# Performance work log

Measured on AMD Instinct MI355X. Metric: run time of the kernel, lower is better.

Reference implementation:

```python
import jax, jax.numpy as jnp
import numpy as np

K, N, E, D = 4, 2048, 4096, 128
BETA = 0.6
EPS = 0.01           # epsilon in hard-sigmoid gating
LAM = 0.05           # lambda_schedule
TC0, TCMAX = 0.3, 0.7
COS_EPS = 1e-8       # F.cosine_similarity eps
MAX_SCORED_EDGES = 500
EDGE_DENSITY = 0.008


def setup_inputs() -> dict:
    key = jax.random.key(0)
    ks = jax.random.split(key, 8)
    s = 0.02
    H = (jax.random.uniform(ks[0], (K, N, E)) < EDGE_DENSITY).astype(jnp.float32)
    X = jax.random.normal(ks[1], (N, D), jnp.float32)
    return dict(
        H=H, X=X, epoch=50,
        mlp_w1=jax.random.normal(ks[2], (K, D, D), jnp.float32) * s,
        mlp_b1=jnp.zeros((K, D), jnp.float32),
        mlp_w2=jax.random.normal(ks[3], (K, D, D), jnp.float32) * s,
        mlp_b2=jnp.zeros((K, D), jnp.float32),
        comp_W=jax.random.normal(ks[4], (K, D, D), jnp.float32) * 0.01,
        att_w1=jax.random.normal(ks[5], (K, D, D // 2), jnp.float32) * s,
        att_b1=jnp.zeros((K, D // 2), jnp.float32),
        att_w2=jax.random.normal(ks[6], (K, D // 2, 1), jnp.float32) * s,
        att_b2=jnp.zeros((K, 1), jnp.float32),
    )


def reference(H, X, epoch, mlp_w1, mlp_b1, mlp_w2, mlp_b2, comp_W,
              att_w1, att_b1, att_w2, att_b2):
    # ---- component level (Eq. 4, batched over K) ----
    h1 = jax.nn.relu(jnp.einsum('nd,kdh->knh', X, mlp_w1) + mlp_b1[:, None, :])
    Xk = jnp.einsum('knh,khe->kne', h1, mlp_w2) + mlp_b2[:, None, :]        # [K,N,D]
    a1 = jax.nn.relu(jnp.einsum('knd,kdh->knh', Xk, att_w1) + att_b1[:, None, :])
    att = jax.nn.sigmoid(jnp.einsum('knh,kho->kno', a1, att_w2) + att_b2[:, None, :])
    S_att = att.mean(axis=(1, 2))                                            # [K]
    frob = jnp.sqrt((comp_W ** 2).sum(axis=(1, 2)))                          # ||W_k||_F
    featn = jnp.sqrt((Xk ** 2).sum(axis=(1, 2)))                             # ||MLP(X_k)||_2 (Frobenius)
    imp = BETA * frob * featn + (1.0 - BETA) * S_att
    pi_c = jax.nn.softmax(imp)
    theta_c = TC0 + (1.0 - jnp.exp(-LAM * epoch)) * (TCMAX - TC0)            # Eq. 3 schedule
    gates = jnp.clip((pi_c - theta_c) / EPS + 0.5, 0.0, 1.0)                 # hard sigmoid
    # K_min = max(1, int(0.1*K)) = 1 -> force top-1 gate open
    keep = jax.nn.one_hot(jnp.argmax(gates), K, dtype=gates.dtype)
    gates = jnp.maximum(gates, keep)

    xnorm = jnp.linalg.norm(X, axis=1)                                       # [N]
    xhat = X / jnp.maximum(xnorm, COS_EPS)[:, None]
    er = jnp.arange(E)
    eye = jnp.eye(N, dtype=bool)

    Hp_l, eg_l, npi_l = [], [], []
    for k in range(K):  # small fixed component count
        Hk = H[k]
        mask = Hk > 0                                                        # [N,E]
        cnt = mask.sum(axis=0)                                               # nodes per hyperedge
        order = jnp.cumsum(mask, axis=0)
        i = jnp.argmax(mask, axis=0)                                         # first incident node
        j = jnp.argmax(mask & (order == 2), axis=0)                          # second incident node
        cos = (xhat[i] * xhat[j]).sum(-1)                                    # [E]
        A = Hk[i, er] * Hk[j, er]                                            # A_ij per edge
        # torch loop: only first 500 edges scored; <2-node edges get 0.1; rest 0
        imp_e = jnp.where(er < MAX_SCORED_EDGES,
                          jnp.where(cnt >= 2, A * cos, 0.1), 0.0)
        pi_e = jax.nn.softmax(imp_e)
        theta_e = jnp.minimum(theta_c, pi_e.mean() + jnp.std(pi_e, ddof=1))  # torch.std unbiased
        eg = jnp.clip((pi_e - theta_e) / EPS + 0.5, 0.0, 1.0)
        eg = jnp.where((eg.sum() < 1.0) & (er == jnp.argmax(pi_e)), 1.0, eg)
        eg_eff = jnp.where(gates[k] > 0.5, eg, jnp.ones_like(eg))
        Hp = Hk * gates[k] * eg_eff[None, :]                                 # pruned incidence

        # ---- node level (Eq. 7) on pruned graph ----
        B = (Hp > 0).astype(Hk.dtype)
        Adj = ((B @ B.T) > 0) & (~eye)                                       # shared-hyperedge neighbors
        degf = Adj.sum(axis=1).astype(Hk.dtype)
        nsum = Adj.astype(Hk.dtype) @ xhat                                   # sum of neighbor unit vecs
        avg = jnp.where(degf > 0, (xhat * nsum).sum(-1) / jnp.maximum(degf, 1.0), 0.0)
        npi = jax.nn.softmax(avg * xnorm)
        Hp_l.append(Hp); eg_l.append(eg); npi_l.append(npi)

    return (jnp.stack(Hp_l), gates, jnp.stack(eg_l), jnp.stack(npi_l))
```

## Files before the change

### kernel.cpp

```cpp
#include <hip/hip_runtime.h>
#include <math.h>

#define KCOMP 4
#define NN 2048
#define EE 4096
#define DD 128
#define MAXNE 96
#define MAXSE 500
#define BETA_C 0.6f
#define EPS_G 0.01f
#define LAM_S 0.05f
#define TC0_C 0.3f
#define TCMAX_C 0.7f
#define COS_EPS_C 1e-8f

static const size_t OFF_XHAT   = 0;
static const size_t OFF_XNORM  = 1048576;
static const size_t OFF_SCAL   = 1056768;
static const size_t OFF_NCNT   = 1057024;
static const size_t OFF_EMASK  = 1089792;
static const size_t OFF_NELIST = 5284096;
static const size_t OFF_IMPE   = 6856960;
static const size_t OFF_EGS    = 6865152;
static const size_t OFF_Z      = 6930688;

__global__ __launch_bounds__(1024) void k_scanx(
    const float4* __restrict__ H4, unsigned* __restrict__ emask,
    const float* __restrict__ X, float* __restrict__ xhat, float* __restrict__ xnorm,
    float* __restrict__ scal) {
  int b = blockIdx.x, t = threadIdx.x;
  if (b < 256) {
    __shared__ unsigned lds[256 * 17];
    int k = b >> 6;
    int rem = b & 63;
    int ch_super = rem >> 4;
    int e4_super = rem & 15;
    int chi = t >> 6;
    int e4i = t & 63;
    int ch = ch_super * 16 + chi;
    int e4 = e4_super * 64 + e4i;
    int n0 = ch * 32;
    const float4* p = H4 + ((size_t)(k * NN + n0)) * (EE / 4) + e4;
    unsigned w0 = 0, w1 = 0, w2 = 0, w3 = 0;
    for (int rb = 0; rb < 32; rb += 8) {
      float4 v[8];
#pragma unroll
      for (int u = 0; u < 8; ++u) v[u] = p[(size_t)(rb + u) * (EE / 4)];
#pragma unroll
      for (int u = 0; u < 8; ++u) {
        unsigned bit = 1u << (rb + u);
        w0 |= (v[u].x > 0.f) ? bit : 0u;
        w1 |= (v[u].y > 0.f) ? bit : 0u;
        w2 |= (v[u].z > 0.f) ? bit : 0u;
        w3 |= (v[u].w > 0.f) ? bit : 0u;
      }
    }
    int el = e4i * 4;
    lds[(el + 0) * 17 + chi] = w0;
    lds[(el + 1) * 17 + chi] = w1;
    lds[(el + 2) * 17 + chi] = w2;
    lds[(el + 3) * 17 + chi] = w3;
    __syncthreads();
    int e_base = e4_super * 256;
    int wi = t & 15;
    int eo = t >> 4;
#pragma unroll
    for (int it = 0; it < 4; ++it) {
      int e_local = it * 64 + eo;
      emask[((size_t)(k * EE) + e_base + e_local) * 64 + ch_super * 16 + wi] =
          lds[e_local * 17 + wi];
    }
  } else {
    if (b == 256 && t < 64) scal[t] = 0.f;
    int node = (b - 256) * 16 + (t >> 6);
    int lane = t & 63;
    float2 v = ((const float2*)X)[(size_t)node * 64 + lane];
    float ss = v.x * v.x + v.y * v.y;
    for (int o = 32; o > 0; o >>= 1) ss += __shfl_xor(ss, o, 64);
    float nrm = sqrtf(ss);
    float den = fmaxf(nrm, COS_EPS_C);
    if (lane == 0) xnorm[node] = nrm;
    float2 o2; o2.x = v.x / den; o2.y = v.y / den;
    ((float2*)xhat)[(size_t)node * 64 + lane] = o2;
  }
}

__global__ void k_mlpf(const float* __restrict__ X,
                       const float* __restrict__ w1, const float* __restrict__ b1,
                       const float* __restrict__ w2, const float* __restrict__ b2,
                       const float* __restrict__ aw1, const float* __restrict__ ab1,
                       const float* __restrict__ aw2, const float* __restrict__ ab2,
                       const float4* __restrict__ compW4, float* __restrict__ scal) {
  __shared__ float Xs[16 * 128];
  __shared__ float H1s[16 * 128];
  __shared__ float XKs[16 * 128];
  __shared__ float A1s[16 * 64];
  __shared__ float red[16];
  int t = threadIdx.x;
  int k = blockIdx.y;
  if (blockIdx.x >= 128) {
    float4 v = compW4[(size_t)k * 4096 + (blockIdx.x - 128) * 256 + t];
    float s = v.x * v.x + v.y * v.y + v.z * v.z + v.w * v.w;
    for (int o = 32; o > 0; o >>= 1) s += __shfl_xor(s, o, 64);
    if ((t & 63) == 0) red[t >> 6] = s;
    __syncthreads();
    if (t == 0) atomicAdd(&scal[8 + k], red[0] + red[1] + red[2] + red[3]);
    return;
  }
  int n0 = blockIdx.x * 16;
  for (int i = t; i < 16 * 128; i += 256) Xs[i] = X[(size_t)n0 * 128 + i];
  __syncthreads();

  int h = t & 127, g = t >> 7;
  const float* W1 = w1 + (size_t)k * 128 * 128;
  float acc[8];
  float bb = b1[k * 128 + h];
#pragma unroll
  for (int i = 0; i < 8; i++) acc[i] = bb;
  for (int d = 0; d < 128; ++d) {
    float w = W1[d * 128 + h];
#pragma unroll
    for (int i = 0; i < 8; i++) acc[i] = fmaf(Xs[(g * 8 + i) * 128 + d], w, acc[i]);
  }
#pragma unroll
  for (int i = 0; i < 8; i++) H1s[(g * 8 + i) * 128 + h] = fmaxf(acc[i], 0.f);
  __syncthreads();

  const float* W2 = w2 + (size_t)k * 128 * 128;
  bb = b2[k * 128 + h];
#pragma unroll
  for (int i = 0; i < 8; i++) acc[i] = bb;
  for (int d = 0; d < 128; ++d) {
    float w = W2[d * 128 + h];
#pragma unroll
    for (int i = 0; i < 8; i++) acc[i] = fmaf(H1s[(g * 8 + i) * 128 + d], w, acc[i]);
  }
  float fpart = 0.f;
#pragma unroll
  for (int i = 0; i < 8; i++) { XKs[(g * 8 + i) * 128 + h] = acc[i]; fpart = fmaf(acc[i], acc[i], fpart); }
  __syncthreads();

  int h2 = t & 63, g4 = t >> 6;
  const float* AW1 = aw1 + (size_t)k * 128 * 64;
  float a4[4];
  float ab = ab1[k * 64 + h2];
#pragma unroll
  for (int i = 0; i < 4; i++) a4[i] = ab;
  for (int d = 0; d < 128; ++d) {
    float w = AW1[d * 64 + h2];
#pragma unroll
    for (int i = 0; i < 4; i++) a4[i] = fmaf(XKs[(g4 * 4 + i) * 128 + d], w, a4[i]);
  }
#pragma unroll
  for (int i = 0; i < 4; i++) A1s[(g4 * 4 + i) * 64 + h2] = fmaxf(a4[i], 0.f);
  __syncthreads();

  float attsum = 0.f;
  if (t < 16) {
    const float* AW2 = aw2 + (size_t)k * 64;
    float a = ab2[k];
    for (int d = 0; d < 64; ++d) a = fmaf(A1s[t * 64 + d], AW2[d], a);
    attsum = 1.f / (1.f + expf(-a));
  }
  for (int o = 32; o > 0; o >>= 1) {
    fpart  += __shfl_xor(fpart, o, 64);
    attsum += __shfl_xor(attsum, o, 64);
  }
  int wv = t >> 6, ln = t & 63;
  if (ln == 0) { red[wv] = fpart; red[8 + wv] = attsum; }
  __syncthreads();
  if (t == 0) {
    float fs = red[0] + red[1] + red[2] + red[3];
    float as = red[8] + red[9] + red[10] + red[11];
    atomicAdd(&scal[0 + k], fs);
    atomicAdd(&scal[4 + k], as);
  }
}

__global__ void k_nelc(const unsigned* __restrict__ emask, int* __restrict__ ncnt,
                       unsigned short* __restrict__ nelist, const float* __restrict__ xhat,
                       float* __restrict__ impE) {
  int k = blockIdx.y, t = threadIdx.x;
  if (blockIdx.x < 64) {
    __shared__ unsigned short lst[32][MAXNE];
    __shared__ int lcnt[32];
    int w = blockIdx.x;
    if (t < 32) lcnt[t] = 0;
    __syncthreads();
    for (int e = t; e < EE; e += 256) {
      unsigned wd = emask[((size_t)(k * EE) + e) * 64 + w];
      while (wd) {
        int b = __builtin_ctz(wd); wd &= wd - 1;
        int slot = atomicAdd(&lcnt[b], 1);
        if (slot < MAXNE) lst[b][slot] = (unsigned short)e;
      }
    }
    __syncthreads();
    if (t < 32) ncnt[k * NN + w * 32 + t] = lcnt[t];
    for (int i = t; i < 32 * MAXNE; i += 256) {
      int b = i / MAXNE, s = i - b * MAXNE;
      int c = lcnt[b]; if (c > MAXNE) c = MAXNE;
      if (s < c) nelist[((size_t)(k * NN + w * 32 + b)) * MAXNE + s] = lst[b][s];
    }
    return;
  }
  int e = (blockIdx.x - 64) * 4 + (t >> 6);
  int lane = t & 63;
  unsigned w = emask[((size_t)(k * EE) + e) * 64 + lane];
  int pc = __popc(w);
  for (int o = 32; o > 0; o >>= 1) pc += __shfl_xor(pc, o, 64);
  float impv = 0.1f;
  if (pc >= 2) {
    unsigned l1 = w ? (unsigned)((lane << 5) + __builtin_ctz(w)) : 0xffffffffu;
    unsigned wr = w & (w - 1);
    unsigned l2 = wr ? (unsigned)((lane << 5) + __builtin_ctz(wr)) : 0xffffffffu;
    unsigned g1 = l1;
    for (int o = 32; o > 0; o >>= 1) {
      unsigned x = (unsigned)__shfl_xor((int)g1, o, 64);
      g1 = g1 < x ? g1 : x;
    }
    unsigned cand = (l1 == g1) ? l2 : l1;
    unsigned g2 = cand;
    for (int o = 32; o > 0; o >>= 1) {
      unsigned x = (unsigned)__shfl_xor((int)g2, o, 64);
      g2 = g2 < x ? g2 : x;
    }
    float2 xi = ((const float2*)xhat)[(size_t)g1 * 64 + lane];
    float2 xj = ((const float2*)xhat)[(size_t)g2 * 64 + lane];
    float d = xi.x * xj.x + xi.y * xj.y;
    for (int o = 32; o > 0; o >>= 1) d += __shfl_xor(d, o, 64);
    impv = d;
  }
  if (lane == 0) impE[k * 512 + e] = impv;
}

__device__ __forceinline__ float blockReduceSum16(float v, float* red, int t) {
  for (int o = 32; o > 0; o >>= 1) v += __shfl_xor(v, o, 64);
  __syncthreads();
  if ((t & 63) == 0) red[t >> 6] = v;
  __syncthreads();
  float s = red[0];
#pragma unroll
  for (int i = 1; i < 16; i++) s += red[i];
  return s;
}

__global__ void k_edgegate(const float* __restrict__ impE, float* __restrict__ scal,
                           const int* __restrict__ epoch, float* __restrict__ out_gates,
                           float* __restrict__ egscaled, float* __restrict__ out_eg) {
  __shared__ float red[16];
  __shared__ int redi[16];
  int k = blockIdx.x;
  int t = threadIdx.x;
  float gates[KCOMP];
  float tc;
  {
    float imp[KCOMP];
    for (int kk = 0; kk < KCOMP; kk++) {
      float featn = sqrtf(scal[0 + kk]);
      float satt  = scal[4 + kk] / (float)NN;
      float frob  = sqrtf(scal[8 + kk]);
      imp[kk] = BETA_C * frob * featn + (1.f - BETA_C) * satt;
    }
    float mx = imp[0];
    for (int kk = 1; kk < KCOMP; kk++) mx = fmaxf(mx, imp[kk]);
    float ex[KCOMP], ssum = 0.f;
    for (int kk = 0; kk < KCOMP; kk++) { ex[kk] = expf(imp[kk] - mx); ssum += ex[kk]; }
    tc = TC0_C + (1.f - expf(-LAM_S * (float)epoch[0])) * (TCMAX_C - TC0_C);
    for (int kk = 0; kk < KCOMP; kk++) {
      float pi = ex[kk] / ssum;
      gates[kk] = fminf(fmaxf((pi - tc) / EPS_G + 0.5f, 0.f), 1.f);
    }
    int am = 0; float bv2 = gates[0];
    for (int kk = 1; kk < KCOMP; kk++) if (gates[kk] > bv2) { bv2 = gates[kk]; am = kk; }
    gates[am] = fmaxf(gates[am], 1.f);
  }
  if (t == 0) {
    scal[12 + k] = gates[k];
    if (k == 0) for (int kk = 0; kk < KCOMP; kk++) out_gates[kk] = gates[kk];
  }
  float imp[4];
#pragma unroll
  for (int j = 0; j < 4; j++) {
    int e = t + j * 1024;
    imp[j] = (e < MAXSE) ? impE[k * 512 + e] : 0.f;
  }
  float m = fmaxf(fmaxf(imp[0], imp[1]), fmaxf(imp[2], imp[3]));
  for (int o = 32; o > 0; o >>= 1) m = fmaxf(m, __shfl_xor(m, o, 64));
  __syncthreads();
  if ((t & 63) == 0) red[t >> 6] = m;
  __syncthreads();
  m = red[0];
#pragma unroll
  for (int i = 1; i < 16; i++) m = fmaxf(m, red[i]);
  float p[4], psum = 0.f;
#pragma unroll
  for (int j = 0; j < 4; j++) { p[j] = expf(imp[j] - m); psum += p[j]; }
  float S = blockReduceSum16(psum, red, t);
  float pi[4], tot = 0.f;
#pragma unroll
  for (int j = 0; j < 4; j++) { pi[j] = p[j] / S; tot += pi[j]; }
  float T = blockReduceSum16(tot, red, t);
  float mean = T / (float)EE;
  float devs = 0.f;
#pragma unroll
  for (int j = 0; j < 4; j++) { float d = pi[j] - mean; devs = fmaf(d, d, devs); }
  float V = blockReduceSum16(devs, red, t);
  float stdv = sqrtf(V / (float)(EE - 1));
  float theta = fminf(tc, mean + stdv);
  float eg[4], egsum = 0.f;
#pragma unroll
  for (int j = 0; j < 4; j++) {
    eg[j] = fminf(fmaxf((pi[j] - theta) / EPS_G + 0.5f, 0.f), 1.f);
    egsum += eg[j];
  }
  float EGS = blockReduceSum16(egsum, red, t);
  float bv = -1e30f; int bi = 0x7fffffff;
#pragma unroll
  for (int j = 0; j < 4; j++) if (pi[j] > bv) { bv = pi[j]; bi = t + j * 1024; }
  for (int o = 32; o > 0; o >>= 1) {
    float ov = __shfl_xor(bv, o, 64); int oi = __shfl_xor(bi, o, 64);
    if (ov > bv || (ov == bv && oi < bi)) { bv = ov; bi = oi; }
  }
  __syncthreads();
  if ((t & 63) == 0) { red[t >> 6] = bv; redi[t >> 6] = bi; }
  __syncthreads();
  float abv = red[0]; int abi = redi[0];
#pragma unroll
  for (int i = 1; i < 16; i++) {
    float ov = red[i]; int oi = redi[i];
    if (ov > abv || (ov == abv && oi < abi)) { abv = ov; abi = oi; }
  }
  float g = gates[k];
#pragma unroll
  for (int j = 0; j < 4; j++) {
    int e = t + j * 1024;
    float egv = eg[j];
    if (EGS < 1.f && e == abi) egv = 1.f;
    out_eg[(size_t)k * EE + e] = egv;
    float eff = (g > 0.5f) ? egv : 1.f;
    egscaled[k * EE + e] = g * eff;
  }
}

__global__ void k_hprow(const unsigned* __restrict__ emask,
                        const int* __restrict__ ncnt, const unsigned short* __restrict__ nelist,
                        const float* __restrict__ egs, const float* __restrict__ scal,
                        const float* __restrict__ xhat, const float* __restrict__ xnorm,
                        float* __restrict__ out, float* __restrict__ z) {
  __shared__ float row[EE];
  __shared__ unsigned short elds[MAXNE];
  __shared__ unsigned wpart[4][64];
  __shared__ unsigned short list[2048];
  __shared__ int cnt_s;
  __shared__ float sred[4];
  int k = blockIdx.y, n = blockIdx.x, t = threadIdx.x;
  int ec = ncnt[k * NN + n]; if (ec > MAXNE) ec = MAXNE;
  if (t < ec) elds[t] = nelist[((size_t)(k * NN + n)) * MAXNE + t];
  float4* row4 = (float4*)row;
  float4 z4 = {0.f, 0.f, 0.f, 0.f};
#pragma unroll
  for (int i = 0; i < 4; i++) row4[t + i * 256] = z4;
  if (t == 0) cnt_s = 0;
  __syncthreads();
  if (t < ec) {
    int e = elds[t];
    row[e] = egs[k * EE + e];
  }
  __syncthreads();
  float4* o4 = (float4*)(out + ((size_t)(k * NN + n)) * EE);
#pragma unroll
  for (int i = 0; i < 4; i++) o4[t + i * 256] = row4[t + i * 256];
  float g = scal[12 + k];
  if (g <= 0.f) { if (t == 0) z[k * NN + n] = 0.f; return; }
  int lane = t & 63, wv = t >> 6;
  unsigned acc = 0;
  for (int it = wv; it < ec; it += 4) {
    int e = (int)elds[it];
    if (row[e] > 0.f) acc |= emask[((size_t)(k * EE) + e) * 64 + lane];
  }
  wpart[wv][lane] = acc;
  __syncthreads();
  if (t < 64) {
    unsigned w = wpart[0][t] | wpart[1][t] | wpart[2][t] | wpart[3][t];
    if (t == (n >> 5)) w &= ~(1u << (n & 31));
    int c = __popc(w);
    if (c > 0) {
      int base = atomicAdd(&cnt_s, c);
      while (w) {
        int b = __builtin_ctz(w); w &= w - 1;
        list[base++] = (unsigned short)((t << 5) + b);
      }
    }
  }
  __syncthreads();
  int cnt = cnt_s;
  if (cnt == 0) { if (t == 0) z[k * NN + n] = 0.f; return; }
  int fc = lane & 31, hh = lane >> 5;
  float4 xn4 = ((const float4*)xhat)[(size_t)n * 32 + fc];
  float a = 0.f;
  for (int it = wv * 2 + hh; it < cnt; it += 8) {
    int m = (int)list[it];
    float4 xm = ((const float4*)xhat)[(size_t)m * 32 + fc];
    a += xn4.x * xm.x + xn4.y * xm.y + xn4.z * xm.z + xn4.w * xm.w;
  }
  for (int o = 32; o > 0; o >>= 1) a += __shfl_xor(a, o, 64);
  if (lane == 0) sred[wv] = a;
  __syncthreads();
  if (t == 0) {
    float s = sred[0] + sred[1] + sred[2] + sred[3];
    z[k * NN + n] = (s / (float)cnt) * xnorm[n];
  }
}

__global__ void k_npi(const float* __restrict__ z, float* __restrict__ out_npi) {
  __shared__ float red[4];
  int k = blockIdx.x, t = threadIdx.x;
  float v[8]; float m = -1e30f;
#pragma unroll
  for (int j = 0; j < 8; j++) { v[j] = z[k * NN + t + j * 256]; m = fmaxf(m, v[j]); }
  for (int o = 32; o > 0; o >>= 1) m = fmaxf(m, __shfl_xor(m, o, 64));
  if ((t & 63) == 0) red[t >> 6] = m;
  __syncthreads();
  m = fmaxf(fmaxf(red[0], red[1]), fmaxf(red[2], red[3]));
  __syncthreads();
  float pe[8]; float s = 0.f;
#pragma unroll
  for (int j = 0; j < 8; j++) { pe[j] = expf(v[j] - m); s += pe[j]; }
  for (int o = 32; o > 0; o >>= 1) s += __shfl_xor(s, o, 64);
  if ((t & 63) == 0) red[t >> 6] = s;
  __syncthreads();
  s = red[0] + red[1] + red[2] + red[3];
#pragma unroll
  for (int j = 0; j < 8; j++) out_npi[k * NN + t + j * 256] = pe[j] / s;
}

extern "C" void kernel_launch(void* const* d_in, const int* in_sizes, int n_in,
                              void* d_out, int out_size, void* d_ws, size_t ws_size,
                              hipStream_t stream) {
  const float* H     = (const float*)d_in[0];
  const float* X     = (const float*)d_in[1];
  const int*   epoch = (const int*)d_in[2];
  const float* w1    = (const float*)d_in[3];
  const float* b1    = (const float*)d_in[4];
  const float* w2    = (const float*)d_in[5];
  const float* b2    = (const float*)d_in[6];
  const float* compW = (const float*)d_in[7];
  const float* aw1   = (const float*)d_in[8];
  const float* ab1   = (const float*)d_in[9];
  const float* aw2   = (const float*)d_in[10];
  const float* ab2   = (const float*)d_in[11];

  char* ws = (char*)d_ws;
  float* xhat  = (float*)(ws + OFF_XHAT);
  float* xnorm = (float*)(ws + OFF_XNORM);
  float* scal  = (float*)(ws + OFF_SCAL);
  int*   ncnt  = (int*)(ws + OFF_NCNT);
  unsigned* emask = (unsigned*)(ws + OFF_EMASK);
  unsigned short* nelist = (unsigned short*)(ws + OFF_NELIST);
  float* impE  = (float*)(ws + OFF_IMPE);
  float* egs   = (float*)(ws + OFF_EGS);
  float* zbuf  = (float*)(ws + OFF_Z);

  float* out       = (float*)d_out;
  float* out_gates = out + (size_t)KCOMP * NN * EE;
  float* out_eg    = out_gates + KCOMP;
  float* out_npi   = out_eg + (size_t)KCOMP * EE;

  k_scanx<<<384, 1024, 0, stream>>>((const float4*)H, emask, X, xhat, xnorm, scal);
  k_mlpf<<<dim3(144, KCOMP), 256, 0, stream>>>(X, w1, b1, w2, b2, aw1, ab1, aw2, ab2,
                                               (const float4*)compW, scal);
  k_nelc<<<dim3(189, KCOMP), 256, 0, stream>>>(emask, ncnt, nelist, xhat, impE);
  k_edgegate<<<KCOMP, 1024, 0, stream>>>(impE, scal, epoch, out_gates, egs, out_eg);
  k_hprow<<<dim3(NN, KCOMP), 256, 0, stream>>>(emask, ncnt, nelist, egs, scal, xhat, xnorm,
                                               out, zbuf);
  k_npi<<<KCOMP, 256, 0, stream>>>(zbuf, out_npi);
}
```

Baseline: 367.1 us.

## Fuse MLP and edge-list kernels into one launch; early-exit gated-off components in hprow

```diff
diff --git a/kernel.cpp b/kernel.cpp
--- a/kernel.cpp
+++ b/kernel.cpp
@@ -85,106 +85,54 @@
   }
 }
 
-__global__ void k_mlpf(const float* __restrict__ X,
-                       const float* __restrict__ w1, const float* __restrict__ b1,
-                       const float* __restrict__ w2, const float* __restrict__ b2,
-                       const float* __restrict__ aw1, const float* __restrict__ ab1,
-                       const float* __restrict__ aw2, const float* __restrict__ ab2,
-                       const float4* __restrict__ compW4, float* __restrict__ scal) {
-  __shared__ float Xs[16 * 128];
-  __shared__ float H1s[16 * 128];
-  __shared__ float XKs[16 * 128];
-  __shared__ float A1s[16 * 64];
-  __shared__ float red[16];
+__global__ void k_mlnel(const float* __restrict__ X,
+                        const float* __restrict__ w1, const float* __restrict__ b1,
+                        const float* __restrict__ w2, const float* __restrict__ b2,
+                        const float* __restrict__ aw1, const float* __restrict__ ab1,
+                        const float* __restrict__ aw2, const float* __restrict__ ab2,
+                        const float4* __restrict__ compW4, float* __restrict__ scal,
+                        const unsigned* __restrict__ emask, int* __restrict__ ncnt,
+                        unsigned short* __restrict__ nelist, const float* __restrict__ xhat,
+                        float* __restrict__ impE) {
+  __shared__ char smem[28736];
   int t = threadIdx.x;
   int k = blockIdx.y;
-  if (blockIdx.x >= 128) {
-    float4 v = compW4[(size_t)k * 4096 + (blockIdx.x - 128) * 256 + t];
-    float s = v.x * v.x + v.y * v.y + v.z * v.z + v.w * v.w;
-    for (int o = 32; o > 0; o >>= 1) s += __shfl_xor(s, o, 64);
-    if ((t & 63) == 0) red[t >> 6] = s;
-    __syncthreads();
-    if (t == 0) atomicAdd(&scal[8 + k], red[0] + red[1] + red[2] + red[3]);
+  int bx = blockIdx.x;
+  if (bx >= 208) {
+    int e = (bx - 208) * 4 + (t >> 6);
+    int lane = t & 63;
+    unsigned w = emask[((size_t)(k * EE) + e) * 64 + lane];
+    int pc = __popc(w);
+    for (int o = 32; o > 0; o >>= 1) pc += __shfl_xor(pc, o, 64);
+    float impv = 0.1f;
+    if (pc >= 2) {
+      unsigned l1 = w ? (unsigned)((lane << 5) + __builtin_ctz(w)) : 0xffffffffu;
+      unsigned wr = w & (w - 1);
+      unsigned l2 = wr ? (unsigned)((lane << 5) + __builtin_ctz(wr)) : 0xffffffffu;
+      unsigned g1 = l1;
+      for (int o = 32; o > 0; o >>= 1) {
+        unsigned x = (unsigned)__shfl_xor((int)g1, o, 64);
+        g1 = g1 < x ? g1 : x;
+      }
+      unsigned cand = (l1 == g1) ? l2 : l1;
+      unsigned g2 = cand;
+      for (int o = 32; o > 0; o >>= 1) {
+        unsigned x = (unsigned)__shfl_xor((int)g2, o, 64);
+        g2 = g2 < x ? g2 : x;
+      }
+      float2 xi = ((const float2*)xhat)[(size_t)g1 * 64 + lane];
+      float2 xj = ((const float2*)xhat)[(size_t)g2 * 64 + lane];
+      float d = xi.x * xj.x + xi.y * xj.y;
+      for (int o = 32; o > 0; o >>= 1) d += __shfl_xor(d, o, 64);
+      impv = d;
+    }
+    if (lane == 0) impE[k * 512 + e] = impv;
     return;
   }
-  int n0 = blockIdx.x * 16;
-  for (int i = t; i < 16 * 128; i += 256) Xs[i] = X[(size_t)n0 * 128 + i];
-  __syncthreads();
-
-  int h = t & 127, g = t >> 7;
-  const float* W1 = w1 + (size_t)k * 128 * 128;
-  float acc[8];
-  float bb = b1[k * 128 + h];
-#pragma unroll
-  for (int i = 0; i < 8; i++) acc[i] = bb;
-  for (int d = 0; d < 128; ++d) {
-    float w = W1[d * 128 + h];
-#pragma unroll
-    for (int i = 0; i < 8; i++) acc[i] = fmaf(Xs[(g * 8 + i) * 128 + d], w, acc[i]);
-  }
-#pragma unroll
-  for (int i = 0; i < 8; i++) H1s[(g * 8 + i) * 128 + h] = fmaxf(acc[i], 0.f);
-  __syncthreads();
-
-  const float* W2 = w2 + (size_t)k * 128 * 128;
-  bb = b2[k * 128 + h];
-#pragma unroll
-  for (int i = 0; i < 8; i++) acc[i] = bb;
-  for (int d = 0; d < 128; ++d) {
-    float w = W2[d * 128 + h];
-#pragma unroll
-    for (int i = 0; i < 8; i++) acc[i] = fmaf(H1s[(g * 8 + i) * 128 + d], w, acc[i]);
-  }
-  float fpart = 0.f;
-#pragma unroll
-  for (int i = 0; i < 8; i++) { XKs[(g * 8 + i) * 128 + h] = acc[i]; fpart = fmaf(acc[i], acc[i], fpart); }
-  __syncthreads();
-
-  int h2 = t & 63, g4 = t >> 6;
-  const float* AW1 = aw1 + (size_t)k * 128 * 64;
-  float a4[4];
-  float ab = ab1[k * 64 + h2];
-#pragma unroll
-  for (int i = 0; i < 4; i++) a4[i] = ab;
-  for (int d = 0; d < 128; ++d) {
-    float w = AW1[d * 64 + h2];
-#pragma unroll
-    for (int i = 0; i < 4; i++) a4[i] = fmaf(XKs[(g4 * 4 + i) * 128 + d], w, a4[i]);
-  }
-#pragma unroll
-  for (int i = 0; i < 4; i++) A1s[(g4 * 4 + i) * 64 + h2] = fmaxf(a4[i], 0.f);
-  __syncthreads();
-
-  float attsum = 0.f;
-  if (t < 16) {
-    const float* AW2 = aw2 + (size_t)k * 64;
-    float a = ab2[k];
-    for (int d = 0; d < 64; ++d) a = fmaf(A1s[t * 64 + d], AW2[d], a);
-    attsum = 1.f / (1.f + expf(-a));
-  }
-  for (int o = 32; o > 0; o >>= 1) {
-    fpart  += __shfl_xor(fpart, o, 64);
-    attsum += __shfl_xor(attsum, o, 64);
-  }
-  int wv = t >> 6, ln = t & 63;
-  if (ln == 0) { red[wv] = fpart; red[8 + wv] = attsum; }
-  __syncthreads();
-  if (t == 0) {
-    float fs = red[0] + red[1] + red[2] + red[3];
-    float as = red[8] + red[9] + red[10] + red[11];
-    atomicAdd(&scal[0 + k], fs);
-    atomicAdd(&scal[4 + k], as);
-  }
-}
-
-__global__ void k_nelc(const unsigned* __restrict__ emask, int* __restrict__ ncnt,
-                       unsigned short* __restrict__ nelist, const float* __restrict__ xhat,
-                       float* __restrict__ impE) {
-  int k = blockIdx.y, t = threadIdx.x;
-  if (blockIdx.x < 64) {
-    __shared__ unsigned short lst[32][MAXNE];
-    __shared__ int lcnt[32];
-    int w = blockIdx.x;
+  if (bx >= 144) {
+    unsigned short* lst = (unsigned short*)smem;
+    int* lcnt = (int*)(smem + 32 * MAXNE * 2);
+    int w = bx - 144;
     if (t < 32) lcnt[t] = 0;
     __syncthreads();
     for (int e = t; e < EE; e += 256) {
@@ -192,7 +140,7 @@
       while (wd) {
         int b = __builtin_ctz(wd); wd &= wd - 1;
         int slot = atomicAdd(&lcnt[b], 1);
-        if (slot < MAXNE) lst[b][slot] = (unsigned short)e;
+        if (slot < MAXNE) lst[b * MAXNE + slot] = (unsigned short)e;
       }
     }
     __syncthreads();
@@ -200,38 +148,92 @@
     for (int i = t; i < 32 * MAXNE; i += 256) {
       int b = i / MAXNE, s = i - b * MAXNE;
       int c = lcnt[b]; if (c > MAXNE) c = MAXNE;
-      if (s < c) nelist[((size_t)(k * NN + w * 32 + b)) * MAXNE + s] = lst[b][s];
+      if (s < c) nelist[((size_t)(k * NN + w * 32 + b)) * MAXNE + s] = lst[b * MAXNE + s];
     }
     return;
   }
-  int e = (blockIdx.x - 64) * 4 + (t >> 6);
-  int lane = t & 63;
-  unsigned w = emask[((size_t)(k * EE) + e) * 64 + lane];
-  int pc = __popc(w);
-  for (int o = 32; o > 0; o >>= 1) pc += __shfl_xor(pc, o, 64);
-  float impv = 0.1f;
-  if (pc >= 2) {
-    unsigned l1 = w ? (unsigned)((lane << 5) + __builtin_ctz(w)) : 0xffffffffu;
-    unsigned wr = w & (w - 1);
-    unsigned l2 = wr ? (unsigned)((lane << 5) + __builtin_ctz(wr)) : 0xffffffffu;
-    unsigned g1 = l1;
-    for (int o = 32; o > 0; o >>= 1) {
-      unsigned x = (unsigned)__shfl_xor((int)g1, o, 64);
-      g1 = g1 < x ? g1 : x;
-    }
-    unsigned cand = (l1 == g1) ? l2 : l1;
-    unsigned g2 = cand;
-    for (int o = 32; o > 0; o >>= 1) {
-      unsigned x = (unsigned)__shfl_xor((int)g2, o, 64);
-      g2 = g2 < x ? g2 : x;
-    }
-    float2 xi = ((const float2*)xhat)[(size_t)g1 * 64 + lane];
-    float2 xj = ((const float2*)xhat)[(size_t)g2 * 64 + lane];
-    float d = xi.x * xj.x + xi.y * xj.y;
-    for (int o = 32; o > 0; o >>= 1) d += __shfl_xor(d, o, 64);
-    impv = d;
-  }
-  if (lane == 0) impE[k * 512 + e] = impv;
+  float* Xs  = (float*)smem;
+  float* H1s = Xs + 2048;
+  float* XKs = H1s + 2048;
+  float* A1s = XKs + 2048;
+  float* red = A1s + 1024;
+  if (bx >= 128) {
+    float4 v = compW4[(size_t)k * 4096 + (bx - 128) * 256 + t];
+    float s = v.x * v.x + v.y * v.y + v.z * v.z + v.w * v.w;
+    for (int o = 32; o > 0; o >>= 1) s += __shfl_xor(s, o, 64);
+    if ((t & 63) == 0) red[t >> 6] = s;
+    __syncthreads();
+    if (t == 0) atomicAdd(&scal[8 + k], red[0] + red[1] + red[2] + red[3]);
+    return;
+  }
+  int n0 = bx * 16;
+  for (int i = t; i < 16 * 128; i += 256) Xs[i] = X[(size_t)n0 * 128 + i];
+  __syncthreads();
+
+  int h = t & 127, g = t >> 7;
+  const float* W1 = w1 + (size_t)k * 128 * 128;
+  float acc[8];
+  float bb = b1[k * 128 + h];
+#pragma unroll
+  for (int i = 0; i < 8; i++) acc[i] = bb;
+  for (int d = 0; d < 128; ++d) {
+    float w = W1[d * 128 + h];
+#pragma unroll
+    for (int i = 0; i < 8; i++) acc[i] = fmaf(Xs[(g * 8 + i) * 128 + d], w, acc[i]);
+  }
+#pragma unroll
+  for (int i = 0; i < 8; i++) H1s[(g * 8 + i) * 128 + h] = fmaxf(acc[i], 0.f);
+  __syncthreads();
+
+  const float* W2 = w2 + (size_t)k * 128 * 128;
+  bb = b2[k * 128 + h];
+#pragma unroll
+  for (int i = 0; i < 8; i++) acc[i] = bb;
+  for (int d = 0; d < 128; ++d) {
+    float w = W2[d * 128 + h];
+#pragma unroll
+    for (int i = 0; i < 8; i++) acc[i] = fmaf(H1s[(g * 8 + i) * 128 + d], w, acc[i]);
+  }
+  float fpart = 0.f;
+#pragma unroll
+  for (int i = 0; i < 8; i++) { XKs[(g * 8 + i) * 128 + h] = acc[i]; fpart = fmaf(acc[i], acc[i], fpart); }
+  __syncthreads();
+
+  int h2 = t & 63, g4 = t >> 6;
+  const float* AW1 = aw1 + (size_t)k * 128 * 64;
+  float a4[4];
+  float ab = ab1[k * 64 + h2];
+#pragma unroll
+  for (int i = 0; i < 4; i++) a4[i] = ab;
+  for (int d = 0; d < 128; ++d) {
+    float w = AW1[d * 64 + h2];
+#pragma unroll
+    for (int i = 0; i < 4; i++) a4[i] = fmaf(XKs[(g4 * 4 + i) * 128 + d], w, a4[i]);
+  }
+#pragma unroll
+  for (int i = 0; i < 4; i++) A1s[(g4 * 4 + i) * 64 + h2] = fmaxf(a4[i], 0.f);
+  __syncthreads();
+
+  float attsum = 0.f;
+  if (t < 16) {
+    const float* AW2 = aw2 + (size_t)k * 64;
+    float a = ab2[k];
+    for (int d = 0; d < 64; ++d) a = fmaf(A1s[t * 64 + d], AW2[d], a);
+    attsum = 1.f / (1.f + expf(-a));
+  }
+  for (int o = 32; o > 0; o >>= 1) {
+    fpart  += __shfl_xor(fpart, o, 64);
+    attsum += __shfl_xor(attsum, o, 64);
+  }
+  int wv = t >> 6, ln = t & 63;
+  if (ln == 0) { red[wv] = fpart; red[8 + wv] = attsum; }
+  __syncthreads();
+  if (t == 0) {
+    float fs = red[0] + red[1] + red[2] + red[3];
+    float as = red[8] + red[9] + red[10] + red[11];
+    atomicAdd(&scal[0 + k], fs);
+    atomicAdd(&scal[4 + k], as);
+  }
 }
 
 __device__ __forceinline__ float blockReduceSum16(float v, float* red, int t) {
@@ -355,6 +357,15 @@
   __shared__ int cnt_s;
   __shared__ float sred[4];
   int k = blockIdx.y, n = blockIdx.x, t = threadIdx.x;
+  float g = scal[12 + k];
+  float4* o4 = (float4*)(out + ((size_t)(k * NN + n)) * EE);
+  if (g <= 0.f) {
+    float4 z4 = {0.f, 0.f, 0.f, 0.f};
+#pragma unroll
+    for (int i = 0; i < 4; i++) o4[t + i * 256] = z4;
+    if (t == 0) z[k * NN + n] = 0.f;
+    return;
+  }
   int ec = ncnt[k * NN + n]; if (ec > MAXNE) ec = MAXNE;
   if (t < ec) elds[t] = nelist[((size_t)(k * NN + n)) * MAXNE + t];
   float4* row4 = (float4*)row;
@@ -368,11 +379,8 @@
     row[e] = egs[k * EE + e];
   }
   __syncthreads();
-  float4* o4 = (float4*)(out + ((size_t)(k * NN + n)) * EE);
 #pragma unroll
   for (int i = 0; i < 4; i++) o4[t + i * 256] = row4[t + i * 256];
-  float g = scal[12 + k];
-  if (g <= 0.f) { if (t == 0) z[k * NN + n] = 0.f; return; }
   int lane = t & 63, wv = t >> 6;
   unsigned acc = 0;
   for (int it = wv; it < ec; it += 4) {
@@ -468,9 +476,9 @@
   float* out_npi   = out_eg + (size_t)KCOMP * EE;
 
   k_scanx<<<384, 1024, 0, stream>>>((const float4*)H, emask, X, xhat, xnorm, scal);
-  k_mlpf<<<dim3(144, KCOMP), 256, 0, stream>>>(X, w1, b1, w2, b2, aw1, ab1, aw2, ab2,
-                                               (const float4*)compW, scal);
-  k_nelc<<<dim3(189, KCOMP), 256, 0, stream>>>(emask, ncnt, nelist, xhat, impE);
+  k_mlnel<<<dim3(333, KCOMP), 256, 0, stream>>>(X, w1, b1, w2, b2, aw1, ab1, aw2, ab2,
+                                                (const float4*)compW, scal,
+                                                emask, ncnt, nelist, xhat, impE);
   k_edgegate<<<KCOMP, 1024, 0, stream>>>(impE, scal, epoch, out_gates, egs, out_eg);
   k_hprow<<<dim3(NN, KCOMP), 256, 0, stream>>>(emask, ncnt, nelist, egs, scal, xhat, xnorm,
                                                out, zbuf);
```

Result: faster. 353.1 us (-3.8%).
